# Kernel optimization log

Hardware: AMD Instinct MI355X
Metric: run time of the kernel (lower is better)

Reference implementation:

```python
import jax, jax.numpy as jnp
import numpy as np

N_OUT = 4096
N_IN = 4096
N_SPARSE = 1024  # int(0.25 * N_IN)
BATCH, SEQ = 4, 2048


def setup_inputs() -> dict:
    key = jax.random.key(0)
    k1, k2, k3 = jax.random.split(key, 3)
    x = jax.random.normal(k1, (BATCH, SEQ, N_IN), dtype=jnp.float32)
    sparse_values = jax.random.normal(k2, (N_OUT, N_SPARSE), dtype=jnp.float32)
    # static equivalent of the boolean sparse_mask: sorted unique column indices
    sparse_idx = jnp.sort(jax.random.permutation(k3, N_IN)[:N_SPARSE]).astype(jnp.int64)
    return {"x": x, "sparse_values": sparse_values, "sparse_idx": sparse_idx}


def reference(x, sparse_values, sparse_idx):
    # x[..., mask] @ sparse_values.T  ->  gather columns then GEMM
    x_g = jnp.take(x, sparse_idx, axis=-1)          # [B, S, n_sparse]
    return jnp.einsum('bsk,ok->bso', x_g, sparse_values)  # [B, S, n_out]
```

## Files before the change

kernel.cpp:

```cpp
#include <hip/hip_runtime.h>
#include <hip/hip_bf16.h>

#define NOUT  4096
#define KDIM  1024
#define MROWS 8192

typedef __attribute__((ext_vector_type(8))) short bf16x8;
typedef __attribute__((ext_vector_type(16))) float f32x16;

__device__ __forceinline__ unsigned short f2bf(float f) {
  union { float f; unsigned int u; } c; c.f = f;
  unsigned int lsb = (c.u >> 16) & 1u;
  c.u += 0x7fffu + lsb;
  return (unsigned short)(c.u >> 16);
}

__device__ __forceinline__ void gload_lds16(const void* g, void* l) {
  __builtin_amdgcn_global_load_lds(
      (const __attribute__((address_space(1))) void*)g,
      (__attribute__((address_space(3))) void*)l, 16, 0, 0);
}

#define FENCE() asm volatile("" ::: "memory")
#define BAR() do { FENCE(); __builtin_amdgcn_s_barrier(); FENCE(); } while (0)
#define VMW(n) asm volatile("s_waitcnt vmcnt(" #n ")" ::: "memory")

__global__ __launch_bounds__(512) void prep(const float* __restrict__ x,
                                            const void* __restrict__ idx_raw,
                                            const float* __restrict__ w,
                                            unsigned short* __restrict__ xg,
                                            unsigned short* __restrict__ wb) {
  __shared__ float rows[16384];
  __shared__ int sidx[1024];
  const int b = blockIdx.x;
  const int t = threadIdx.x;

  if (b < 2048) {
    const long long* p64 = (const long long*)idx_raw;
    const int* p32 = (const int*)idx_raw;
    const bool is64 = ((unsigned long long)p64[0]) < 4096ull;
    const float* src = x + (size_t)b * 4 * 4096;
#pragma unroll
    for (int i = 0; i < 8; ++i)
      ((float4*)rows)[t + 512 * i] = ((const float4*)src)[t + 512 * i];
    if (is64) {
      sidx[t] = (int)p64[t];
      sidx[t + 512] = (int)p64[t + 512];
    } else {
      sidx[t] = p32[t];
      sidx[t + 512] = p32[t + 512];
    }
    __syncthreads();
    ushort4* dst = (ushort4*)(xg + (size_t)b * 4 * 1024);
#pragma unroll
    for (int i = 0; i < 2; ++i) {
      const int q = t + 512 * i;
      const int e = 4 * q;
      const int rbase = (e >> 10) * 4096;
      const int k = e & 1023;
      ushort4 o;
      o.x = f2bf(rows[rbase + sidx[k + 0]]);
      o.y = f2bf(rows[rbase + sidx[k + 1]]);
      o.z = f2bf(rows[rbase + sidx[k + 2]]);
      o.w = f2bf(rows[rbase + sidx[k + 3]]);
      dst[q] = o;
    }
  } else {
    const int i0 = (b - 2048) * 2048 + t;
#pragma unroll
    for (int j = 0; j < 4; ++j) {
      float4 v = ((const float4*)w)[i0 + 512 * j];
      ushort4 o;
      o.x = f2bf(v.x); o.y = f2bf(v.y); o.z = f2bf(v.z); o.w = f2bf(v.w);
      ((ushort4*)wb)[i0 + 512 * j] = o;
    }
  }
}

__global__ __launch_bounds__(256, 4) void gemm128(const unsigned short* __restrict__ A,
                                                  const unsigned short* __restrict__ B,
                                                  float* __restrict__ C) {
  __shared__ __align__(16) unsigned short lds[16384];

  const int tid = threadIdx.x;
  const int lane = tid & 63;
  const int wid = tid >> 6;
  const int wm = wid >> 1, wn = wid & 1;
  const int l31 = lane & 31, lh = lane >> 5;

  const int bid = blockIdx.x;
  const int swz = (bid & 7) * 256 + (bid >> 3);
  const int bm0 = (swz >> 5) * 128;
  const int bn0 = (swz & 31) * 128;

  const int rS = tid >> 2;
  const int cS = (tid & 3) ^ ((tid >> 3) & 3);
  const unsigned short* Ag = A + (size_t)(bm0 + rS) * KDIM + cS * 8;
  const unsigned short* Bg = B + (size_t)(bn0 + rS) * KDIM + cS * 8;
  const int tid8 = tid * 8;

  const int sw = (l31 >> 1) & 3;
  const int cK0 = (lh ^ sw) * 8;
  const int cK1 = cK0 ^ 16;
  const int aOff = (wm * 64 + l31) * 32;
  const int bOff = 4096 + (wn * 64 + l31) * 32;

  f32x16 acc[2][2] = {};

#define STAGE(d, t) do {                                              \
    unsigned short* Lb = lds + (d) * 8192;                            \
    gload_lds16(Ag + (t) * 32,              Lb + tid8);               \
    gload_lds16(Ag + 64 * KDIM + (t) * 32,  Lb + 2048 + tid8);        \
    gload_lds16(Bg + (t) * 32,              Lb + 4096 + tid8);        \
    gload_lds16(Bg + 64 * KDIM + (t) * 32,  Lb + 6144 + tid8);        \
  } while (0)

  STAGE(0, 0);

  for (int t = 0; t < 32; ++t) {
    const int d = t & 1;
    if (t < 31) {
      STAGE(d ^ 1, t + 1);
      VMW(4);
    } else {
      VMW(0);
    }
    BAR();
    const unsigned short* La = lds + d * 8192;
    bf16x8 b0[2], b1[2];
    b0[0] = *(const bf16x8*)(La + bOff + cK0);
    b0[1] = *(const bf16x8*)(La + bOff + cK1);
    b1[0] = *(const bf16x8*)(La + bOff + 1024 + cK0);
    b1[1] = *(const bf16x8*)(La + bOff + 1024 + cK1);
    __builtin_amdgcn_s_setprio(1);
#pragma unroll
    for (int mf = 0; mf < 2; ++mf) {
      bf16x8 a0 = *(const bf16x8*)(La + aOff + mf * 1024 + cK0);
      bf16x8 a1 = *(const bf16x8*)(La + aOff + mf * 1024 + cK1);
      acc[mf][0] = __builtin_amdgcn_mfma_f32_32x32x16_bf16(a0, b0[0], acc[mf][0], 0, 0, 0);
      acc[mf][0] = __builtin_amdgcn_mfma_f32_32x32x16_bf16(a1, b0[1], acc[mf][0], 0, 0, 0);
      acc[mf][1] = __builtin_amdgcn_mfma_f32_32x32x16_bf16(a0, b1[0], acc[mf][1], 0, 0, 0);
      acc[mf][1] = __builtin_amdgcn_mfma_f32_32x32x16_bf16(a1, b1[1], acc[mf][1], 0, 0, 0);
    }
    __builtin_amdgcn_s_setprio(0);
    BAR();
  }
#undef STAGE

  float* base = C + (size_t)(bm0 + wm * 64) * NOUT + bn0 + wn * 64;
#pragma unroll
  for (int mf = 0; mf < 2; ++mf)
#pragma unroll
    for (int nf = 0; nf < 2; ++nf) {
      f32x16 v = acc[mf][nf];
#pragma unroll
      for (int r = 0; r < 16; ++r) {
        const int rowi = mf * 32 + (r & 3) + 8 * (r >> 2) + 4 * lh;
        base[(size_t)rowi * NOUT + nf * 32 + l31] = v[r];
      }
    }
}

extern "C" void kernel_launch(void* const* d_in, const int* in_sizes, int n_in,
                              void* d_out, int out_size, void* d_ws, size_t ws_size,
                              hipStream_t stream) {
  const float* x   = (const float*)d_in[0];
  const float* sv  = (const float*)d_in[1];
  const void*  idx = d_in[2];
  float* out = (float*)d_out;

  unsigned short* xg = (unsigned short*)d_ws;
  unsigned short* wb = xg + (size_t)MROWS * KDIM;

  prep<<<2560, 512, 0, stream>>>(x, idx, sv, xg, wb);

  gemm128<<<2048, 256, 0, stream>>>(xg, wb, out);
}
```

Baseline: 138.3 us.

## Enlarge GEMM tile to 256x256 with 1024-thread blocks and K-step 64

Replaces the 128x128-tile, 256-thread GEMM with a 256x256-tile, 16-wave block that stages 64-wide K slices into a 128KB double-buffered LDS region with a new XOR swizzle. The goal is to halve global/L2 traffic per output and halve the number of barrier-separated iterations. In exchange it limits occupancy to one block per CU, removes the L2-friendly block swizzle, and yields only 512 blocks for the whole GPU.

```diff
diff --git a/kernel.cpp b/kernel.cpp
--- a/kernel.cpp
+++ b/kernel.cpp
@@ -77,70 +77,80 @@
   }
 }
 
-__global__ __launch_bounds__(256, 4) void gemm128(const unsigned short* __restrict__ A,
+__global__ __launch_bounds__(1024, 4) void gemm1k(const unsigned short* __restrict__ A,
                                                   const unsigned short* __restrict__ B,
                                                   float* __restrict__ C) {
-  __shared__ __align__(16) unsigned short lds[16384];
+  __shared__ __align__(16) unsigned short lds[65536];
 
   const int tid = threadIdx.x;
   const int lane = tid & 63;
   const int wid = tid >> 6;
-  const int wm = wid >> 1, wn = wid & 1;
+  const int wm = wid >> 2, wn = wid & 3;
   const int l31 = lane & 31, lh = lane >> 5;
 
-  const int bid = blockIdx.x;
-  const int swz = (bid & 7) * 256 + (bid >> 3);
-  const int bm0 = (swz >> 5) * 128;
-  const int bn0 = (swz & 31) * 128;
+  const int bn0 = blockIdx.x * 256;
+  const int bm0 = blockIdx.y * 256;
 
-  const int rS = tid >> 2;
-  const int cS = (tid & 3) ^ ((tid >> 3) & 3);
-  const unsigned short* Ag = A + (size_t)(bm0 + rS) * KDIM + cS * 8;
-  const unsigned short* Bg = B + (size_t)(bn0 + rS) * KDIM + cS * 8;
+  const int pr = tid >> 3;
+  const int cg = (tid & 7) ^ (pr & 7) ^ ((pr >> 3) & 3);
+  const unsigned short* Ag = A + (size_t)(bm0 + pr) * KDIM + cg * 8;
+  const unsigned short* Bg = B + (size_t)(bn0 + pr) * KDIM + cg * 8;
   const int tid8 = tid * 8;
 
-  const int sw = (l31 >> 1) & 3;
-  const int cK0 = (lh ^ sw) * 8;
+  const int sw8 = (l31 & 7) ^ (l31 >> 3);
+  const int cK0 = (lh ^ sw8) * 8;
   const int cK1 = cK0 ^ 16;
-  const int aOff = (wm * 64 + l31) * 32;
-  const int bOff = 4096 + (wn * 64 + l31) * 32;
+  const int cK2 = cK0 ^ 32;
+  const int cK3 = cK0 ^ 48;
+  const int aOff = wm * 4096 + l31 * 64;
+  const int bOff = 16384 + wn * 4096 + l31 * 64;
 
   f32x16 acc[2][2] = {};
 
-#define STAGE(d, t) do {                                              \
-    unsigned short* Lb = lds + (d) * 8192;                            \
-    gload_lds16(Ag + (t) * 32,              Lb + tid8);               \
-    gload_lds16(Ag + 64 * KDIM + (t) * 32,  Lb + 2048 + tid8);        \
-    gload_lds16(Bg + (t) * 32,              Lb + 4096 + tid8);        \
-    gload_lds16(Bg + 64 * KDIM + (t) * 32,  Lb + 6144 + tid8);        \
+#define STAGE(d, t) do {                                                \
+    unsigned short* Lb = lds + (d) * 32768;                             \
+    gload_lds16(Ag + (t) * 64,                        Lb + tid8);       \
+    gload_lds16(Ag + (size_t)128 * KDIM + (t) * 64,   Lb + 8192 + tid8);  \
+    gload_lds16(Bg + (t) * 64,                        Lb + 16384 + tid8); \
+    gload_lds16(Bg + (size_t)128 * KDIM + (t) * 64,   Lb + 24576 + tid8); \
   } while (0)
 
   STAGE(0, 0);
 
-  for (int t = 0; t < 32; ++t) {
+  for (int t = 0; t < 16; ++t) {
     const int d = t & 1;
-    if (t < 31) {
+    if (t < 15) {
       STAGE(d ^ 1, t + 1);
       VMW(4);
     } else {
       VMW(0);
     }
     BAR();
-    const unsigned short* La = lds + d * 8192;
-    bf16x8 b0[2], b1[2];
+    const unsigned short* La = lds + d * 32768;
+    bf16x8 a0[4], a1[4], b0[4], b1[4];
+    a0[0] = *(const bf16x8*)(La + aOff + cK0);
+    a0[1] = *(const bf16x8*)(La + aOff + cK1);
+    a0[2] = *(const bf16x8*)(La + aOff + cK2);
+    a0[3] = *(const bf16x8*)(La + aOff + cK3);
+    a1[0] = *(const bf16x8*)(La + aOff + 2048 + cK0);
+    a1[1] = *(const bf16x8*)(La + aOff + 2048 + cK1);
+    a1[2] = *(const bf16x8*)(La + aOff + 2048 + cK2);
+    a1[3] = *(const bf16x8*)(La + aOff + 2048 + cK3);
     b0[0] = *(const bf16x8*)(La + bOff + cK0);
     b0[1] = *(const bf16x8*)(La + bOff + cK1);
-    b1[0] = *(const bf16x8*)(La + bOff + 1024 + cK0);
-    b1[1] = *(const bf16x8*)(La + bOff + 1024 + cK1);
+    b0[2] = *(const bf16x8*)(La + bOff + cK2);
+    b0[3] = *(const bf16x8*)(La + bOff + cK3);
+    b1[0] = *(const bf16x8*)(La + bOff + 2048 + cK0);
+    b1[1] = *(const bf16x8*)(La + bOff + 2048 + cK1);
+    b1[2] = *(const bf16x8*)(La + bOff + 2048 + cK2);
+    b1[3] = *(const bf16x8*)(La + bOff + 2048 + cK3);
     __builtin_amdgcn_s_setprio(1);
 #pragma unroll
-    for (int mf = 0; mf < 2; ++mf) {
-      bf16x8 a0 = *(const bf16x8*)(La + aOff + mf * 1024 + cK0);
-      bf16x8 a1 = *(const bf16x8*)(La + aOff + mf * 1024 + cK1);
-      acc[mf][0] = __builtin_amdgcn_mfma_f32_32x32x16_bf16(a0, b0[0], acc[mf][0], 0, 0, 0);
-      acc[mf][0] = __builtin_amdgcn_mfma_f32_32x32x16_bf16(a1, b0[1], acc[mf][0], 0, 0, 0);
-      acc[mf][1] = __builtin_amdgcn_mfma_f32_32x32x16_bf16(a0, b1[0], acc[mf][1], 0, 0, 0);
-      acc[mf][1] = __builtin_amdgcn_mfma_f32_32x32x16_bf16(a1, b1[1], acc[mf][1], 0, 0, 0);
+    for (int kb = 0; kb < 4; ++kb) {
+      acc[0][0] = __builtin_amdgcn_mfma_f32_32x32x16_bf16(a0[kb], b0[kb], acc[0][0], 0, 0, 0);
+      acc[0][1] = __builtin_amdgcn_mfma_f32_32x32x16_bf16(a0[kb], b1[kb], acc[0][1], 0, 0, 0);
+      acc[1][0] = __builtin_amdgcn_mfma_f32_32x32x16_bf16(a1[kb], b0[kb], acc[1][0], 0, 0, 0);
+      acc[1][1] = __builtin_amdgcn_mfma_f32_32x32x16_bf16(a1[kb], b1[kb], acc[1][1], 0, 0, 0);
     }
     __builtin_amdgcn_s_setprio(0);
     BAR();
@@ -174,5 +184,6 @@
 
   prep<<<2560, 512, 0, stream>>>(x, idx, sv, xg, wb);
 
-  gemm128<<<2048, 256, 0, stream>>>(xg, wb, out);
+  dim3 grid(NOUT / 256, MROWS / 256);
+  gemm1k<<<grid, 1024, 0, stream>>>(xg, wb, out);
 }
```

Result: slower. 269.3 us (+94.8%).
